# Optimization experiments

Measured on AMD Instinct MI355X. Metric: run time of the kernel, lower is better.

## Reference

```python
import jax, jax.numpy as jnp
import numpy as np

N_NODES = 50000


def gcn_conv(x, W, b, src, dst, n):
    """PyG GCNConv: add self-loops, symmetric deg^-1/2 normalization, then aggregate."""
    loop = jnp.arange(n, dtype=src.dtype)
    s = jnp.concatenate([src, loop])  # [E+N]
    d = jnp.concatenate([dst, loop])  # [E+N]
    deg = jax.ops.segment_sum(jnp.ones_like(d, dtype=x.dtype), d, num_segments=n)  # [N]
    dinv = jnp.where(deg > 0, jax.lax.rsqrt(deg), 0.0)
    h = x @ W  # transform first (reduces message width), [N, out]
    norm = (dinv[s] * dinv[d])[:, None]  # [E+N, 1]
    msgs = h[s] * norm  # gather + scale, [E+N, out]
    out = jax.ops.segment_sum(msgs, d, num_segments=n)  # scatter-add, [N, out]
    return out + b


def setup_inputs() -> dict:
    key = jax.random.key(0)
    k1, k2, k3, k4 = jax.random.split(key, 4)
    in_dim, hidden, n_cls = 512, 256, 64
    x = jax.random.normal(k1, (N_NODES, in_dim), dtype=jnp.float32)
    edge_index = jax.random.randint(k2, (2, 800000), 0, N_NODES, dtype=jnp.int64)
    W1 = jax.random.normal(k3, (in_dim, hidden), dtype=jnp.float32) / np.sqrt(in_dim)
    b1 = jnp.zeros((hidden,), dtype=jnp.float32)
    W2 = jax.random.normal(k4, (hidden, n_cls), dtype=jnp.float32) / np.sqrt(hidden)
    b2 = jnp.zeros((n_cls,), dtype=jnp.float32)
    return {"x": x, "edge_index": edge_index, "W1": W1, "b1": b1, "W2": W2, "b2": b2}


def reference(x, edge_index, W1, b1, W2, b2):
    src, dst = edge_index[0], edge_index[1]
    n = x.shape[0]
    h = jax.nn.relu(gcn_conv(x, W1, b1, src, dst, n))  # dropout is identity in eval mode
    logits = gcn_conv(h, W2, b2, src, dst, n)
    evidence = jax.nn.softplus(logits)
    return (evidence, h)
```

## Files before the change

### kernel.cpp

```cpp
#include <hip/hip_runtime.h>


#define N_NODES 50000
#define IN_DIM 512
#define HID 256
#define NCLS 64

typedef unsigned short u16;
typedef unsigned int u32;
typedef __attribute__((ext_vector_type(8))) short short8;
typedef __attribute__((ext_vector_type(4))) float float4_t;

__device__ __forceinline__ float bf_lo(u32 v) {
    u32 u = v << 16; float f; __builtin_memcpy(&f, &u, 4); return f;
}
__device__ __forceinline__ float bf_hi(u32 v) {
    u32 u = v & 0xffff0000u; float f; __builtin_memcpy(&f, &u, 4); return f;
}
__device__ __forceinline__ u16 f2bf(float f) {
    u32 u; __builtin_memcpy(&u, &f, 4);
    return (u16)((u + 0x7fffu + ((u >> 16) & 1u)) >> 16);
}
__device__ __forceinline__ void add8(float* acc, uint4 v) {
    acc[0] += bf_lo(v.x); acc[1] += bf_hi(v.x);
    acc[2] += bf_lo(v.y); acc[3] += bf_hi(v.y);
    acc[4] += bf_lo(v.z); acc[5] += bf_hi(v.z);
    acc[6] += bf_lo(v.w); acc[7] += bf_hi(v.w);
}
__device__ __forceinline__ void acc8(float* acc, uint4 v, float w) {
    acc[0] += w * bf_lo(v.x); acc[1] += w * bf_hi(v.x);
    acc[2] += w * bf_lo(v.y); acc[3] += w * bf_hi(v.y);
    acc[4] += w * bf_lo(v.z); acc[5] += w * bf_hi(v.z);
    acc[6] += w * bf_lo(v.w); acc[7] += w * bf_hi(v.w);
}

__global__ void init_kernel(int* __restrict__ cnt, int* __restrict__ cursor, int n) {
    int i = blockIdx.x * blockDim.x + threadIdx.x;
    if (i < n) { cnt[i] = 0; cursor[i] = 0; }
}

__global__ void count_kernel(const int* __restrict__ dst, int* __restrict__ cnt, int E) {
    int e = blockIdx.x * blockDim.x + threadIdx.x;
    if (e < E) atomicAdd(&cnt[dst[e]], 1);
}

__global__ __launch_bounds__(256) void s1_kernel(const int* __restrict__ cnt,
                                                 int* __restrict__ blocksum,
                                                 float* __restrict__ dinv, int n) {
    int tid = threadIdx.x;
    int i = blockIdx.x * 256 + tid;
    int c = (i < n) ? cnt[i] : 0;
    if (i < n) dinv[i] = rsqrtf((float)(c + 1));
    __shared__ int s[256];
    s[tid] = c;
    __syncthreads();
    for (int off = 128; off > 0; off >>= 1) {
        if (tid < off) s[tid] += s[tid + off];
        __syncthreads();
    }
    if (tid == 0) blocksum[blockIdx.x] = s[0];
}

__global__ __launch_bounds__(256) void s3_kernel(const int* __restrict__ cnt,
                                                 const int* __restrict__ blocksum,
                                                 int* __restrict__ row_ptr, int n, int nb) {
    __shared__ int bs[256];
    __shared__ int s[256];
    int tid = threadIdx.x;
    int v = (tid < nb) ? blocksum[tid] : 0;
    bs[tid] = v;
    __syncthreads();
    for (int off = 1; off < 256; off <<= 1) {
        int a = (tid >= off) ? bs[tid - off] : 0;
        __syncthreads();
        bs[tid] += a;
        __syncthreads();
    }
    int boff = (blockIdx.x == 0) ? 0 : bs[blockIdx.x - 1];
    int i = blockIdx.x * 256 + tid;
    int c = (i < n) ? cnt[i] : 0;
    s[tid] = c;
    __syncthreads();
    for (int off = 1; off < 256; off <<= 1) {
        int a = (tid >= off) ? s[tid - off] : 0;
        __syncthreads();
        s[tid] += a;
        __syncthreads();
    }
    if (i <= n) row_ptr[i] = boff + s[tid] - c;
}

__global__ void fill_kernel(const int* __restrict__ src, const int* __restrict__ dst,
                            const int* __restrict__ row_ptr, int* __restrict__ cursor,
                            int* __restrict__ csr_src, int E) {
    int e = blockIdx.x * blockDim.x + threadIdx.x;
    if (e >= E) return;
    int d = dst[e];
    int pos = row_ptr[d] + atomicAdd(&cursor[d], 1);
    csr_src[pos] = src[e];
}

__global__ __launch_bounds__(256) void tcast_kernel(const float* __restrict__ W,
                                                    u16* __restrict__ Wt, int K, int N) {
    int idx = blockIdx.x * 256 + threadIdx.x;
    if (idx >= K * N) return;
    int n = idx / K, k = idx - n * K;
    Wt[idx] = f2bf(W[k * N + n]);
}

template <int BM, int BN, int K, int N, bool AF32, bool SCALE>
__global__ __launch_bounds__(256) void mfma_gemm_kernel(const void* __restrict__ Ain,
                                                        const u16* __restrict__ Bt,
                                                        u16* __restrict__ C, int M,
                                                        const float* __restrict__ rowscale) {
    constexpr int WCOLS = (BN >= 128) ? 2 : 1;
    constexpr int WROWS = 4 / WCOLS;
    static_assert(WROWS * 64 == BM && WCOLS * 64 == BN, "wave tiling mismatch");
    constexpr int LDSA = BM * 32;
    __shared__ u16 lds[LDSA + BN * 32];

    const int tid = threadIdx.x;
    const int wave = tid >> 6, lane = tid & 63;
    const int wm = wave / WCOLS, wn = wave % WCOLS;
    const int quad = lane >> 4, l15 = lane & 15;
    const int row0 = blockIdx.y * BM;
    const int col0 = blockIdx.x * BN;

    float4_t acc[4][4];
#pragma unroll
    for (int mi = 0; mi < 4; mi++)
#pragma unroll
        for (int ni = 0; ni < 4; ni++) {
            float4_t z = {0.f, 0.f, 0.f, 0.f};
            acc[mi][ni] = z;
        }

    for (int k0 = 0; k0 < K; k0 += 32) {
#pragma unroll
        for (int i = 0; i < BM / 64; i++) {
            int c = tid + i * 256;
            int r = c >> 2;
            int gr = row0 + r;
            gr = gr < M ? gr : M - 1;
            if constexpr (AF32) {
                const float* gp = (const float*)Ain + (long)gr * K + k0 + (c & 3) * 8;
                float4 p0 = ((const float4*)gp)[0];
                float4 p1 = ((const float4*)gp)[1];
                uint4 o;
                o.x = (u32)f2bf(p0.x) | ((u32)f2bf(p0.y) << 16);
                o.y = (u32)f2bf(p0.z) | ((u32)f2bf(p0.w) << 16);
                o.z = (u32)f2bf(p1.x) | ((u32)f2bf(p1.y) << 16);
                o.w = (u32)f2bf(p1.z) | ((u32)f2bf(p1.w) << 16);
                *(uint4*)(lds + c * 8) = o;
            } else {
                const u16* gp = (const u16*)Ain + (long)gr * K + k0 + (c & 3) * 8;
                u16* lp = lds + c * 8;
                __builtin_amdgcn_global_load_lds((const __attribute__((address_space(1))) u32*)gp,
                                                 (__attribute__((address_space(3))) u32*)lp,
                                                 16, 0, 0);
            }
        }
#pragma unroll
        for (int i = 0; i < BN / 64; i++) {
            int c = tid + i * 256;
            int r = c >> 2;
            const u16* gp = Bt + (long)(col0 + r) * K + k0 + (c & 3) * 8;
            u16* lp = lds + LDSA + c * 8;
            __builtin_amdgcn_global_load_lds((const __attribute__((address_space(1))) u32*)gp,
                                             (__attribute__((address_space(3))) u32*)lp,
                                             16, 0, 0);
        }
        __syncthreads();

        short8 af[4], bfr[4];
#pragma unroll
        for (int mi = 0; mi < 4; mi++)
            af[mi] = *(const short8*)(lds + (wm * 64 + mi * 16 + l15) * 32 + quad * 8);
#pragma unroll
        for (int ni = 0; ni < 4; ni++)
            bfr[ni] = *(const short8*)(lds + LDSA + (wn * 64 + ni * 16 + l15) * 32 + quad * 8);
#pragma unroll
        for (int mi = 0; mi < 4; mi++)
#pragma unroll
            for (int ni = 0; ni < 4; ni++)
                acc[mi][ni] = __builtin_amdgcn_mfma_f32_16x16x32_bf16(af[mi], bfr[ni],
                                                                      acc[mi][ni], 0, 0, 0);
        __syncthreads();
    }

#pragma unroll
    for (int mi = 0; mi < 4; mi++) {
#pragma unroll
        for (int r = 0; r < 4; r++) {
            int row = row0 + wm * 64 + mi * 16 + quad * 4 + r;
            if (row < M) {
                float sc = 1.f;
                if constexpr (SCALE) sc = rowscale[row];
#pragma unroll
                for (int ni = 0; ni < 4; ni++) {
                    int col = col0 + wn * 64 + ni * 16 + l15;
                    C[(long)row * N + col] = f2bf(acc[mi][ni][r] * sc);
                }
            }
        }
    }
}

__global__ __launch_bounds__(256) void agg_wide_kernel(const u16* __restrict__ t,
                                                       const int* __restrict__ row_ptr,
                                                       const int* __restrict__ csr_src,
                                                       const float* __restrict__ dinv,
                                                       const float* __restrict__ bias,
                                                       float* __restrict__ out_f,
                                                       u16* __restrict__ out_bf, int n) {
    constexpr int FEAT = 256;
    int node = (blockIdx.x * blockDim.x + threadIdx.x) >> 6;
    int lane = threadIdx.x & 63;
    if (node >= n) return;
    const int g = lane >> 5;
    const int r = lane & 31;
    float acc[8] = {};
    const int beg = row_ptr[node], end = row_ptr[node + 1];
    int e = beg;
    for (; e + 16 <= end; e += 16) {
        int s[8]; uint4 v[8];
#pragma unroll
        for (int u = 0; u < 8; u++) s[u] = csr_src[e + u * 2 + g];
#pragma unroll
        for (int u = 0; u < 8; u++) v[u] = *(const uint4*)(t + (long)s[u] * FEAT + r * 8);
#pragma unroll
        for (int u = 0; u < 8; u++) add8(acc, v[u]);
    }
    for (; e + 8 <= end; e += 8) {
        int s[4]; uint4 v[4];
#pragma unroll
        for (int u = 0; u < 4; u++) s[u] = csr_src[e + u * 2 + g];
#pragma unroll
        for (int u = 0; u < 4; u++) v[u] = *(const uint4*)(t + (long)s[u] * FEAT + r * 8);
#pragma unroll
        for (int u = 0; u < 4; u++) add8(acc, v[u]);
    }
    for (; e < end; e += 2) {
        int ee = e + g;
        if (ee < end) {
            int s = csr_src[ee];
            uint4 v = *(const uint4*)(t + (long)s * FEAT + r * 8);
            add8(acc, v);
        }
    }
#pragma unroll
    for (int j = 0; j < 8; j++) acc[j] += __shfl_xor(acc[j], 32, 64);

    if (lane < 32) {
        const float di = dinv[node];
        uint4 sv = *(const uint4*)(t + (long)node * FEAT + lane * 8);
        float self[8] = {bf_lo(sv.x), bf_hi(sv.x), bf_lo(sv.y), bf_hi(sv.y),
                         bf_lo(sv.z), bf_hi(sv.z), bf_lo(sv.w), bf_hi(sv.w)};
        float4 b0 = *(const float4*)(bias + lane * 8);
        float4 b1 = *(const float4*)(bias + lane * 8 + 4);
        float bb[8] = {b0.x, b0.y, b0.z, b0.w, b1.x, b1.y, b1.z, b1.w};
        float rv[8];
#pragma unroll
        for (int j = 0; j < 8; j++)
            rv[j] = fmaxf(di * (acc[j] + self[j]) + bb[j], 0.f);
        long base = (long)node * FEAT + lane * 8;
        *(float4*)(out_f + base) = make_float4(rv[0], rv[1], rv[2], rv[3]);
        *(float4*)(out_f + base + 4) = make_float4(rv[4], rv[5], rv[6], rv[7]);
        uint4 o;
        o.x = (u32)f2bf(rv[0]) | ((u32)f2bf(rv[1]) << 16);
        o.y = (u32)f2bf(rv[2]) | ((u32)f2bf(rv[3]) << 16);
        o.z = (u32)f2bf(rv[4]) | ((u32)f2bf(rv[5]) << 16);
        o.w = (u32)f2bf(rv[6]) | ((u32)f2bf(rv[7]) << 16);
        *(uint4*)(out_bf + base) = o;
    }
}

__global__ __launch_bounds__(256) void agg_n8_kernel(const u16* __restrict__ t,
                                                     const int* __restrict__ row_ptr,
                                                     const int* __restrict__ csr_src,
                                                     const float* __restrict__ dinv,
                                                     const float* __restrict__ bias,
                                                     float* __restrict__ out_f, int n) {
    constexpr int FEAT = 64;
    const int wid = (blockIdx.x * blockDim.x + threadIdx.x) >> 6;
    const int lane = threadIdx.x & 63;
    const int g = lane >> 3;
    const int r = lane & 7;
    const int node = wid * 8 + g;
    const bool valid = node < n;
    const int nd = valid ? node : (n - 1);
    const int beg = row_ptr[nd];
    const int deg = valid ? (row_ptr[nd + 1] - beg) : 0;
    float acc[8] = {};
    for (int e = 0;; e += 4) {
        if (!__any(e < deg)) break;
        int s[4]; float w[4]; uint4 v[4];
#pragma unroll
        for (int u = 0; u < 4; u++) {
            bool a = (e + u) < deg;
            s[u] = a ? csr_src[beg + e + u] : 0;
            w[u] = a ? 1.f : 0.f;
        }
#pragma unroll
        for (int u = 0; u < 4; u++) v[u] = *(const uint4*)(t + (long)s[u] * FEAT + r * 8);
#pragma unroll
        for (int u = 0; u < 4; u++) acc8(acc, v[u], w[u]);
    }
    const float di = dinv[nd];
    uint4 sv = *(const uint4*)(t + (long)nd * FEAT + r * 8);
    float self[8] = {bf_lo(sv.x), bf_hi(sv.x), bf_lo(sv.y), bf_hi(sv.y),
                     bf_lo(sv.z), bf_hi(sv.z), bf_lo(sv.w), bf_hi(sv.w)};
    float4 b0 = *(const float4*)(bias + r * 8);
    float4 b1 = *(const float4*)(bias + r * 8 + 4);
    float bb[8] = {b0.x, b0.y, b0.z, b0.w, b1.x, b1.y, b1.z, b1.w};
    float rv[8];
#pragma unroll
    for (int j = 0; j < 8; j++) {
        float v = di * (acc[j] + self[j]) + bb[j];
        rv[j] = fmaxf(v, 0.f) + __logf(1.f + __expf(-fabsf(v)));
    }
    if (valid) {
        long base = (long)nd * FEAT + r * 8;
        *(float4*)(out_f + base) = make_float4(rv[0], rv[1], rv[2], rv[3]);
        *(float4*)(out_f + base + 4) = make_float4(rv[4], rv[5], rv[6], rv[7]);
    }
}

extern "C" void kernel_launch(void* const* d_in, const int* in_sizes, int n_in,
                              void* d_out, int out_size, void* d_ws, size_t ws_size,
                              hipStream_t stream) {
    const float* x  = (const float*)d_in[0];
    const int*   ei = (const int*)d_in[1];
    const float* W1 = (const float*)d_in[2];
    const float* b1 = (const float*)d_in[3];
    const float* W2 = (const float*)d_in[4];
    const float* b2 = (const float*)d_in[5];

    float* evidence = (float*)d_out;
    float* h        = (float*)d_out + (long)N_NODES * NCLS;

    const int E = in_sizes[1] / 2;
    const int* src = ei;
    const int* dst = ei + E;

    const int NB = (N_NODES + 255) / 256;

    char* w = (char*)d_ws;
    int*   cnt      = (int*)w;  w += 50048 * 4;
    int*   cursor   = (int*)w;  w += 50048 * 4;
    int*   row_ptr  = (int*)w;  w += 50064 * 4;
    float* dinv     = (float*)w; w += 50048 * 4;
    int*   blocksum = (int*)w;  w += 256 * 4;
    int*   csr_src  = (int*)w;  w += 800000 * 4;
    u16*   hbf      = (u16*)w;  w += (long)N_NODES * IN_DIM * 2;
    u16*   w1t      = (u16*)w;  w += IN_DIM * HID * 2;
    u16*   w2t      = (u16*)w;  w += HID * NCLS * 2;
    u16*   t1bf     = (u16*)w;  w += (long)N_NODES * HID * 2;
    u16*   t2bf     = t1bf;

    init_kernel<<<NB, 256, 0, stream>>>(cnt, cursor, N_NODES);
    count_kernel<<<(E + 255) / 256, 256, 0, stream>>>(dst, cnt, E);
    s1_kernel<<<NB, 256, 0, stream>>>(cnt, blocksum, dinv, N_NODES);
    s3_kernel<<<NB, 256, 0, stream>>>(cnt, blocksum, row_ptr, N_NODES, NB);
    fill_kernel<<<(E + 255) / 256, 256, 0, stream>>>(src, dst, row_ptr, cursor, csr_src, E);

    tcast_kernel<<<(IN_DIM * HID + 255) / 256, 256, 0, stream>>>(W1, w1t, IN_DIM, HID);
    tcast_kernel<<<(HID * NCLS + 255) / 256, 256, 0, stream>>>(W2, w2t, HID, NCLS);

    {
        dim3 grid(HID / 128, (N_NODES + 127) / 128);
        mfma_gemm_kernel<128, 128, IN_DIM, HID, true, true>
            <<<grid, 256, 0, stream>>>(x, w1t, t1bf, N_NODES, dinv);
    }
    agg_wide_kernel<<<(N_NODES * 64 + 255) / 256, 256, 0, stream>>>(
        t1bf, row_ptr, csr_src, dinv, b1, h, hbf, N_NODES);

    {
        dim3 grid(NCLS / 64, (N_NODES + 255) / 256);
        mfma_gemm_kernel<256, 64, HID, NCLS, false, true>
            <<<grid, 256, 0, stream>>>(hbf, w2t, t2bf, N_NODES, dinv);
    }
    {
        int waves = (N_NODES + 7) / 8;
        int blocks = (waves + 3) / 4;
        agg_n8_kernel<<<blocks, 256, 0, stream>>>(
            t2bf, row_ptr, csr_src, dinv, b2, evidence, N_NODES);
    }
}
```

Baseline: 406.6 us.

## Double-buffer LDS in MFMA GEMM and shrink second GEMM tile to 64x64

Restructures the GEMM main loop to use two LDS buffers, issuing global loads for the next K-slice before computing on the current one, which halves the barriers per iteration. For the fp32 A path, loads go to registers first and are converted and written to LDS after the MFMAs. The second GEMM now uses a 64x64 tile with a fixed 2x2 wave layout, launching four times as many blocks to improve occupancy across CUs. Doubling LDS and keeping prefetched fp32 data in registers raises register and LDS pressure.

Result: faster. 396.3 us (-2.5%).

```diff
diff --git a/kernel.cpp b/kernel.cpp
--- a/kernel.cpp
+++ b/kernel.cpp
@@ -20,6 +20,9 @@
 __device__ __forceinline__ u16 f2bf(float f) {
     u32 u; __builtin_memcpy(&u, &f, 4);
     return (u16)((u + 0x7fffu + ((u >> 16) & 1u)) >> 16);
+}
+__device__ __forceinline__ u32 pack2bf(float a, float b) {
+    return (u32)f2bf(a) | ((u32)f2bf(b) << 16);
 }
 __device__ __forceinline__ void add8(float* acc, uint4 v) {
     acc[0] += bf_lo(v.x); acc[1] += bf_hi(v.x);
@@ -113,11 +116,19 @@
                                                         const u16* __restrict__ Bt,
                                                         u16* __restrict__ C, int M,
                                                         const float* __restrict__ rowscale) {
-    constexpr int WCOLS = (BN >= 128) ? 2 : 1;
-    constexpr int WROWS = 4 / WCOLS;
-    static_assert(WROWS * 64 == BM && WCOLS * 64 == BN, "wave tiling mismatch");
+    constexpr int WROWS = 2, WCOLS = 2;
+    constexpr int WMR = BM / WROWS;
+    constexpr int WNR = BN / WCOLS;
+    constexpr int MR = WMR / 16;
+    constexpr int NR = WNR / 16;
+    constexpr int AI = BM / 64;
+    constexpr int BI = BN / 64;
     constexpr int LDSA = BM * 32;
-    __shared__ u16 lds[LDSA + BN * 32];
+    constexpr int LDSB = BN * 32;
+    constexpr int LDST = LDSA + LDSB;
+    constexpr int NT = K / 32;
+    static_assert(MR * 16 * WROWS == BM && NR * 16 * WCOLS == BN, "tiling");
+    __shared__ u16 lds[2 * LDST];
 
     const int tid = threadIdx.x;
     const int wave = tid >> 6, lane = tid & 63;
@@ -126,79 +137,119 @@
     const int row0 = blockIdx.y * BM;
     const int col0 = blockIdx.x * BN;
 
-    float4_t acc[4][4];
-#pragma unroll
-    for (int mi = 0; mi < 4; mi++)
-#pragma unroll
-        for (int ni = 0; ni < 4; ni++) {
-            float4_t z = {0.f, 0.f, 0.f, 0.f};
-            acc[mi][ni] = z;
-        }
-
-    for (int k0 = 0; k0 < K; k0 += 32) {
-#pragma unroll
-        for (int i = 0; i < BM / 64; i++) {
+    const float* Af = (const float*)Ain;
+    const u16* Abf = (const u16*)Ain;
+
+    int gra[AI];
+#pragma unroll
+    for (int i = 0; i < AI; i++) {
+        int gr = row0 + ((tid + i * 256) >> 2);
+        gra[i] = gr < M ? gr : M - 1;
+    }
+
+    float4 pa[AI][2];
+
+    auto loadA = [&](int k0) {
+#pragma unroll
+        for (int i = 0; i < AI; i++) {
             int c = tid + i * 256;
-            int r = c >> 2;
-            int gr = row0 + r;
-            gr = gr < M ? gr : M - 1;
-            if constexpr (AF32) {
-                const float* gp = (const float*)Ain + (long)gr * K + k0 + (c & 3) * 8;
-                float4 p0 = ((const float4*)gp)[0];
-                float4 p1 = ((const float4*)gp)[1];
-                uint4 o;
-                o.x = (u32)f2bf(p0.x) | ((u32)f2bf(p0.y) << 16);
-                o.y = (u32)f2bf(p0.z) | ((u32)f2bf(p0.w) << 16);
-                o.z = (u32)f2bf(p1.x) | ((u32)f2bf(p1.y) << 16);
-                o.w = (u32)f2bf(p1.z) | ((u32)f2bf(p1.w) << 16);
-                *(uint4*)(lds + c * 8) = o;
-            } else {
-                const u16* gp = (const u16*)Ain + (long)gr * K + k0 + (c & 3) * 8;
-                u16* lp = lds + c * 8;
-                __builtin_amdgcn_global_load_lds((const __attribute__((address_space(1))) u32*)gp,
-                                                 (__attribute__((address_space(3))) u32*)lp,
-                                                 16, 0, 0);
-            }
-        }
-#pragma unroll
-        for (int i = 0; i < BN / 64; i++) {
+            const float* gp = Af + (long)gra[i] * K + k0 + (c & 3) * 8;
+            pa[i][0] = ((const float4*)gp)[0];
+            pa[i][1] = ((const float4*)gp)[1];
+        }
+    };
+    auto writeA = [&](u16* buf) {
+#pragma unroll
+        for (int i = 0; i < AI; i++) {
+            int c = tid + i * 256;
+            uint4 o;
+            o.x = pack2bf(pa[i][0].x, pa[i][0].y);
+            o.y = pack2bf(pa[i][0].z, pa[i][0].w);
+            o.z = pack2bf(pa[i][1].x, pa[i][1].y);
+            o.w = pack2bf(pa[i][1].z, pa[i][1].w);
+            *(uint4*)(buf + c * 8) = o;
+        }
+    };
+    auto stageA_lds = [&](int k0, u16* buf) {
+#pragma unroll
+        for (int i = 0; i < AI; i++) {
+            int c = tid + i * 256;
+            const u16* gp = Abf + (long)gra[i] * K + k0 + (c & 3) * 8;
+            __builtin_amdgcn_global_load_lds((const __attribute__((address_space(1))) u32*)gp,
+                                             (__attribute__((address_space(3))) u32*)(buf + c * 8),
+                                             16, 0, 0);
+        }
+    };
+    auto stageB = [&](int k0, u16* buf) {
+#pragma unroll
+        for (int i = 0; i < BI; i++) {
             int c = tid + i * 256;
             int r = c >> 2;
             const u16* gp = Bt + (long)(col0 + r) * K + k0 + (c & 3) * 8;
-            u16* lp = lds + LDSA + c * 8;
             __builtin_amdgcn_global_load_lds((const __attribute__((address_space(1))) u32*)gp,
-                                             (__attribute__((address_space(3))) u32*)lp,
+                                             (__attribute__((address_space(3))) u32*)(buf + c * 8),
                                              16, 0, 0);
         }
-        __syncthreads();
-
-        short8 af[4], bfr[4];
-#pragma unroll
-        for (int mi = 0; mi < 4; mi++)
-            af[mi] = *(const short8*)(lds + (wm * 64 + mi * 16 + l15) * 32 + quad * 8);
-#pragma unroll
-        for (int ni = 0; ni < 4; ni++)
-            bfr[ni] = *(const short8*)(lds + LDSA + (wn * 64 + ni * 16 + l15) * 32 + quad * 8);
-#pragma unroll
-        for (int mi = 0; mi < 4; mi++)
-#pragma unroll
-            for (int ni = 0; ni < 4; ni++)
+    };
+
+    float4_t acc[MR][NR];
+#pragma unroll
+    for (int mi = 0; mi < MR; mi++)
+#pragma unroll
+        for (int ni = 0; ni < NR; ni++) {
+            float4_t z = {0.f, 0.f, 0.f, 0.f};
+            acc[mi][ni] = z;
+        }
+
+    if constexpr (AF32) {
+        loadA(0);
+        writeA(lds);
+    } else {
+        stageA_lds(0, lds);
+    }
+    stageB(0, lds + LDSA);
+    __syncthreads();
+
+    for (int t = 0; t < NT; t++) {
+        u16* cur = lds + (t & 1) * LDST;
+        u16* nxt = lds + ((t + 1) & 1) * LDST;
+        const bool pre = (t + 1) < NT;
+        if (pre) {
+            if constexpr (AF32) loadA((t + 1) * 32);
+            else stageA_lds((t + 1) * 32, nxt);
+            stageB((t + 1) * 32, nxt + LDSA);
+        }
+
+        short8 af[MR], bfr[NR];
+#pragma unroll
+        for (int mi = 0; mi < MR; mi++)
+            af[mi] = *(const short8*)(cur + (wm * WMR + mi * 16 + l15) * 32 + quad * 8);
+#pragma unroll
+        for (int ni = 0; ni < NR; ni++)
+            bfr[ni] = *(const short8*)(cur + LDSA + (wn * WNR + ni * 16 + l15) * 32 + quad * 8);
+#pragma unroll
+        for (int mi = 0; mi < MR; mi++)
+#pragma unroll
+            for (int ni = 0; ni < NR; ni++)
                 acc[mi][ni] = __builtin_amdgcn_mfma_f32_16x16x32_bf16(af[mi], bfr[ni],
                                                                       acc[mi][ni], 0, 0, 0);
-        __syncthreads();
-    }
-
-#pragma unroll
-    for (int mi = 0; mi < 4; mi++) {
+        if (pre) {
+            if constexpr (AF32) writeA(nxt);
+        }
+        __syncthreads();
+    }
+
+#pragma unroll
+    for (int mi = 0; mi < MR; mi++) {
 #pragma unroll
         for (int r = 0; r < 4; r++) {
-            int row = row0 + wm * 64 + mi * 16 + quad * 4 + r;
+            int row = row0 + wm * WMR + mi * 16 + quad * 4 + r;
             if (row < M) {
                 float sc = 1.f;
                 if constexpr (SCALE) sc = rowscale[row];
 #pragma unroll
-                for (int ni = 0; ni < 4; ni++) {
-                    int col = col0 + wn * 64 + ni * 16 + l15;
+                for (int ni = 0; ni < NR; ni++) {
+                    int col = col0 + wn * WNR + ni * 16 + l15;
                     C[(long)row * N + col] = f2bf(acc[mi][ni][r] * sc);
                 }
             }
@@ -376,8 +427,8 @@
         t1bf, row_ptr, csr_src, dinv, b1, h, hbf, N_NODES);
 
     {
-        dim3 grid(NCLS / 64, (N_NODES + 255) / 256);
-        mfma_gemm_kernel<256, 64, HID, NCLS, false, true>
+        dim3 grid(NCLS / 64, (N_NODES + 63) / 64);
+        mfma_gemm_kernel<64, 64, HID, NCLS, false, true>
             <<<grid, 256, 0, stream>>>(hbf, w2t, t2bf, N_NODES, dinv);
     }
     {
```
